# Performance work log

Measured on AMD Instinct MI355X. Metric: run time of the kernel, lower is better.

## Reference

```python
import jax, jax.numpy as jnp
import numpy as np

B, N = 1, 512
CS, CZ = 384, 128
H, DQK, DV, PQK, PV = 12, 16, 16, 4, 8
EPS = 1e-8
SW = float(np.sqrt(1.0 / (3 * DQK)))            # scalar_weights
PW = float(np.sqrt(1.0 / (3 * PQK * 9.0 / 2)))  # point_weights
ZW = float(np.sqrt(1.0 / 3))                    # attention_2d_weights


def _lin(key, din, dout):
    return 0.02 * jax.random.normal(key, (din, dout), dtype=jnp.float32), jnp.zeros((dout,), dtype=jnp.float32)


def setup_inputs():
    key = jax.random.key(0)
    ks = jax.random.split(key, 16)
    Wsq, bsq = _lin(ks[0], CS, H * DQK)
    Wsk, bsk = _lin(ks[1], CS, H * DQK)
    Wsv, bsv = _lin(ks[2], CS, H * DV)
    Wsb, bsb = _lin(ks[3], CZ, H)
    Wpq, bpq = _lin(ks[4], CS, H * PQK * 3)
    Wpk, bpk = _lin(ks[5], CS, H * PQK * 3)
    Wpv, bpv = _lin(ks[6], CS, H * PV * 3)
    Wout, bout = _lin(ks[7], H * (DV + PV * 4 + CZ), CS)
    w_attn = 0.5 * jax.random.normal(ks[8], (3,), dtype=jnp.float32)  # attn_linear weight (1,3)
    b_attn = jnp.zeros((), dtype=jnp.float32)
    tpw = jnp.full((H,), float(np.log(np.e - 1.0)), dtype=jnp.float32)  # trainable_point_weight
    s = jax.random.normal(ks[9], (B, N, CS), dtype=jnp.float32)
    z = jax.random.normal(ks[10], (B, N, N, CZ), dtype=jnp.float32)
    rot = jax.random.normal(ks[11], (B, N, 3, 3), dtype=jnp.float32)
    tran = jax.random.normal(ks[12], (B, N, 3), dtype=jnp.float32)
    res_mask = jnp.ones((B, N), dtype=jnp.float32)
    return dict(s=s, z=z, rot=rot, tran=tran, res_mask=res_mask,
                Wsq=Wsq, bsq=bsq, Wsk=Wsk, bsk=bsk, Wsv=Wsv, bsv=bsv,
                Wsb=Wsb, bsb=bsb, Wpq=Wpq, bpq=bpq, Wpk=Wpk, bpk=bpk,
                Wpv=Wpv, bpv=bpv, w_attn=w_attn, b_attn=b_attn, tpw=tpw,
                Wout=Wout, bout=bout)


def _ipa(s, z, rot, tran, res_mask, Wsq, bsq, Wsk, bsk, Wsv, bsv, Wsb, bsb,
         Wpq, bpq, Wpk, bpk, Wpv, bpv, w_attn, b_attn, tpw, Wout, bout):
    b, n, _ = s.shape
    sq = (s @ Wsq + bsq).reshape(b, n, H, DQK)
    sk = (s @ Wsk + bsk).reshape(b, n, H, DQK)
    sv = (s @ Wsv + bsv).reshape(b, n, H, DV)
    sb = z @ Wsb + bsb  # [b, i, j, h] pair bias

    def to_global(W, bias, p):
        t = (s @ W + bias).reshape(b, n, H, p, 3)
        return jnp.einsum('bnxy,bnhpy->bnhpx', rot, t) + tran[:, :, None, None, :]

    pqg = to_global(Wpq, bpq, PQK)
    pkg = to_global(Wpk, bpk, PQK)
    pvg = to_global(Wpv, bpv, PV)

    diff = pqg[:, :, None] - pkg[:, None, :]          # [b, i, j, h, p, 3]
    sdist = jnp.sum(diff * diff, axis=(-1, -2))       # [b, i, j, h]

    attn_point = -0.5 * jax.nn.softplus(tpw) * sdist * PW
    attn_scalar = jnp.einsum('bihd,bjhd->bijh', sq * SW, sk)
    attn_pair = sb * ZW
    # attn_linear(stack([scalar, point, pair], -1)).squeeze(-1)
    logits = attn_scalar * w_attn[0] + attn_point * w_attn[1] + attn_pair * w_attn[2] + b_attn

    mask2d = res_mask[:, :, None] * res_mask[:, None, :]
    logits = jnp.where(mask2d[..., None] == 0, jnp.finfo(logits.dtype).min, logits)
    attn = jax.nn.softmax(logits, axis=2)             # softmax over j

    r_scalar = jnp.einsum('bijh,bjhd->bihd', attn, sv)
    r_pt_g = jnp.einsum('bijh,bjhpc->bihpc', attn, pvg)
    # rotate back to local frame: R^T (x - t)
    r_pt = jnp.einsum('biyx,bihpy->bihpx', rot, r_pt_g - tran[:, :, None, None, :])
    r_norm = jnp.sqrt(jnp.sum(r_pt * r_pt, axis=-1) + EPS)  # [b, i, h, p]
    r_pair = jnp.einsum('bijh,bijc->bihc', attn, z)

    cat = jnp.concatenate([r_scalar, r_pt.reshape(b, n, H, PV * 3), r_norm, r_pair], axis=-1)
    return cat.reshape(b, n, -1) @ Wout + bout


def reference(s, z, rot, tran, res_mask, Wsq, bsq, Wsk, bsk, Wsv, bsv, Wsb, bsb,
              Wpq, bpq, Wpk, bpk, Wpv, bpv, w_attn, b_attn, tpw, Wout, bout):
    return _ipa(s, z, rot, tran, res_mask, Wsq, bsq, Wsk, bsk, Wsv, bsv, Wsb, bsb,
                Wpq, bpq, Wpk, bpk, Wpv, bpv, w_attn, b_attn, tpw, Wout, bout)
```

## Files before the change

### kernel.cpp

```cpp
#include <hip/hip_runtime.h>
#include <hip/hip_bf16.h>
#include <math.h>

#define NN 512
#define CSD 384
#define CZ 128
#define HH 12
#define TMPW 1152
#define CATH 176
#define CATDIM 2112
#define NSPLIT 6
#define KSPL 352

#define SW 0.14433756729740643f
#define PW 0.13608276348795434f
#define ZW 0.57735026918962576f
#define NEG_INF -3.4028234663852886e38f

typedef float f32x4_t __attribute__((ext_vector_type(4)));
typedef short bf16x8_t __attribute__((ext_vector_type(8)));

union BFU { uint4 q; bf16x8_t v; ushort u[8]; };

static __device__ __forceinline__ ushort f2bf(float f) {
    __hip_bfloat16 h = __float2bfloat16(f);
    return *reinterpret_cast<ushort*>(&h);
}
static __device__ __forceinline__ float bf2f(ushort u) {
    unsigned int v = ((unsigned int)u) << 16;
    return __uint_as_float(v);
}

__global__ void proj_gemm_kernel(const float* __restrict__ s, const float* __restrict__ rot,
                                 const float* __restrict__ tran,
                                 const float* __restrict__ Wsq, const float* __restrict__ bsq,
                                 const float* __restrict__ Wsk, const float* __restrict__ bsk,
                                 const float* __restrict__ Wsv, const float* __restrict__ bsv,
                                 const float* __restrict__ Wpq, const float* __restrict__ bpq,
                                 const float* __restrict__ Wpk, const float* __restrict__ bpk,
                                 const float* __restrict__ Wpv, const float* __restrict__ bpv,
                                 float* __restrict__ tmp)
{
    int bx = blockIdx.x;
    int n0 = blockIdx.y * 32;
    int f0 = bx * 48;
    const float* W; const float* bb; int dout; int segstart;
    if (bx < 4)       { W = Wsq; bb = bsq; dout = 192; segstart = 0; }
    else if (bx < 8)  { W = Wsk; bb = bsk; dout = 192; segstart = 192; }
    else if (bx < 12) { W = Wsv; bb = bsv; dout = 192; segstart = 384; }
    else if (bx < 15) { W = Wpq; bb = bpq; dout = 144; segstart = 576; }
    else if (bx < 18) { W = Wpk; bb = bpk; dout = 144; segstart = 720; }
    else              { W = Wpv; bb = bpv; dout = 288; segstart = 864; }
    int colbase = f0 - segstart;

    __shared__ float St[32][34];
    __shared__ float Ws[32][49];
    int tid = threadIdx.x;
    int ty = tid >> 4, tx = tid & 15;
    float acc[2][3] = {{0,0,0},{0,0,0}};

    for (int k0 = 0; k0 < CSD; k0 += 32) {
        {
            int r = tid >> 3, c4 = (tid & 7) * 4;
            float4 v = *(const float4*)&s[(size_t)(n0 + r) * CSD + k0 + c4];
            St[c4 + 0][r] = v.x; St[c4 + 1][r] = v.y; St[c4 + 2][r] = v.z; St[c4 + 3][r] = v.w;
        }
        for (int e = tid; e < 1536; e += 256) {
            int r = e / 48, c = e % 48;
            Ws[r][c] = W[(size_t)(k0 + r) * dout + colbase + c];
        }
        __syncthreads();
        #pragma unroll
        for (int k = 0; k < 32; k++) {
            float2 a = *(const float2*)&St[k][ty * 2];
            float b0 = Ws[k][tx * 3], b1 = Ws[k][tx * 3 + 1], b2 = Ws[k][tx * 3 + 2];
            acc[0][0] += a.x * b0; acc[0][1] += a.x * b1; acc[0][2] += a.x * b2;
            acc[1][0] += a.y * b0; acc[1][1] += a.y * b1; acc[1][2] += a.y * b2;
        }
        __syncthreads();
    }
    float bv0 = bb[colbase + tx * 3], bv1 = bb[colbase + tx * 3 + 1], bv2 = bb[colbase + tx * 3 + 2];
    #pragma unroll
    for (int r = 0; r < 2; r++) {
        int n = n0 + ty * 2 + r;
        float v0 = acc[r][0] + bv0, v1 = acc[r][1] + bv1, v2 = acc[r][2] + bv2;
        float* o = tmp + (size_t)n * TMPW + f0 + tx * 3;
        if (bx >= 12) {
            const float* R = rot + n * 9;
            const float* T = tran + n * 3;
            float g0 = R[0] * v0 + R[1] * v1 + R[2] * v2 + T[0];
            float g1 = R[3] * v0 + R[4] * v1 + R[5] * v2 + T[1];
            float g2 = R[6] * v0 + R[7] * v1 + R[8] * v2 + T[2];
            o[0] = g0; o[1] = g1; o[2] = g2;
        } else {
            o[0] = v0; o[1] = v1; o[2] = v2;
        }
    }
}

__global__ __launch_bounds__(512) void fused_z_kernel(const float* __restrict__ z,
                                                      const float* __restrict__ resm,
                                                      const float* __restrict__ Wsb,
                                                      const float* __restrict__ bsb,
                                                      const float* __restrict__ watt,
                                                      const float* __restrict__ batt,
                                                      const float* __restrict__ tpw,
                                                      const float* __restrict__ tmp,
                                                      ushort* __restrict__ attn_bf,
                                                      float* __restrict__ cat)
{
    int i = blockIdx.x;
    __shared__ float lt[NN * 17];
    __shared__ float sbz[NN * 12];
    __shared__ float sqs[192];
    __shared__ float pqi[144];
    __shared__ float cpt[12];
    __shared__ float cb[12];
    int tid = threadIdx.x;
    int w = tid >> 6, lane = tid & 63;
    int l16 = lane & 15, lhi = lane >> 4;
    float w0 = watt[0], w1 = watt[1], w2 = watt[2], ba = batt[0];
    float A2 = w2 * ZW;

    for (int k = tid; k < 192; k += 512) sqs[k] = tmp[(size_t)i * TMPW + k] * (SW * w0);
    if (tid < 144) pqi[tid] = tmp[(size_t)i * TMPW + 576 + tid];
    if (tid < 12) {
        cpt[tid] = -0.5f * log1pf(expf(tpw[tid])) * PW * w1;
        cb[tid]  = A2 * bsb[tid] + ba;
    }

    BFU breg[4];
    #pragma unroll
    for (int kk = 0; kk < 4; kk++) {
        #pragma unroll
        for (int e = 0; e < 8; e++) {
            int k = kk * 32 + lhi * 8 + e;
            float v = (l16 < HH) ? Wsb[k * HH + l16] * A2 : 0.f;
            breg[kk].u[e] = f2bf(v);
        }
    }

    const float* zi = z + (size_t)i * NN * CZ;
    float4 prA[8], prB[8];
    {
        const float* zr = zi + (size_t)(w * 16 + l16) * CZ + lhi * 8;
        #pragma unroll
        for (int kk = 0; kk < 4; kk++) {
            prA[kk * 2]     = *(const float4*)&zr[kk * 32];
            prA[kk * 2 + 1] = *(const float4*)&zr[kk * 32 + 4];
        }
    }
    #pragma unroll
    for (int t = 0; t < 4; t++) {
        float4* cur = (t & 1) ? prB : prA;
        float4* nxt = (t & 1) ? prA : prB;
        if (t < 3) {
            const float* zr = zi + (size_t)((w + 8 * (t + 1)) * 16 + l16) * CZ + lhi * 8;
            #pragma unroll
            for (int kk = 0; kk < 4; kk++) {
                nxt[kk * 2]     = *(const float4*)&zr[kk * 32];
                nxt[kk * 2 + 1] = *(const float4*)&zr[kk * 32 + 4];
            }
        }
        f32x4_t acc = {0.f, 0.f, 0.f, 0.f};
        #pragma unroll
        for (int kk = 0; kk < 4; kk++) {
            float4 f0 = cur[kk * 2], f1 = cur[kk * 2 + 1];
            BFU a;
            a.u[0] = f2bf(f0.x); a.u[1] = f2bf(f0.y); a.u[2] = f2bf(f0.z); a.u[3] = f2bf(f0.w);
            a.u[4] = f2bf(f1.x); a.u[5] = f2bf(f1.y); a.u[6] = f2bf(f1.z); a.u[7] = f2bf(f1.w);
            acc = __builtin_amdgcn_mfma_f32_16x16x32_bf16(a.v, breg[kk].v, acc, 0, 0, 0);
        }
        if (l16 < HH) {
            int T = w + 8 * t;
            #pragma unroll
            for (int r = 0; r < 4; r++)
                sbz[(T * 16 + lhi * 4 + r) * 12 + l16] = acc[r];
        }
    }
    __syncthreads();

    {
        int jg = tid >> 2, hg = tid & 3, h0 = hg * 3;
        float rmi = resm[i];
        #pragma unroll
        for (int rr = 0; rr < 4; rr++) {
            int j = jg + 128 * rr;
            float mj = rmi * resm[j];
            const float* sbr = &sbz[j * 12 + h0];
            #pragma unroll
            for (int t = 0; t < 3; t++) {
                int h = h0 + t;
                const float4* skp = (const float4*)(tmp + (size_t)j * TMPW + 192 + h * 16);
                const float4* sqp = (const float4*)&sqs[h * 16];
                float d0 = 0.f;
                #pragma unroll
                for (int q = 0; q < 4; q++) {
                    float4 kv = skp[q];
                    float4 qv = sqp[q];
                    d0 += qv.x * kv.x + qv.y * kv.y + qv.z * kv.z + qv.w * kv.w;
                }
                const float4* pkp = (const float4*)(tmp + (size_t)j * TMPW + 720 + h * 12);
                const float4* pqp = (const float4*)&pqi[h * 12];
                float sd = 0.f;
                #pragma unroll
                for (int q = 0; q < 3; q++) {
                    float4 kv = pkp[q];
                    float4 qv = pqp[q];
                    float a = qv.x - kv.x, bb2 = qv.y - kv.y, cc = qv.z - kv.z, e = qv.w - kv.w;
                    sd += a * a + bb2 * bb2 + cc * cc + e * e;
                }
                float lg = cb[h] + sbr[t] + d0 + cpt[h] * sd;
                if (mj == 0.f) lg = NEG_INF;
                lt[j * 17 + h] = lg;
            }
        }
    }
    __syncthreads();

    if (w < 4) {
        #pragma unroll
        for (int t = 0; t < 3; t++) {
            int h = w * 3 + t;
            float v[8]; float m = -INFINITY;
            #pragma unroll
            for (int u = 0; u < 8; u++) { v[u] = lt[(lane + 64 * u) * 17 + h]; m = fmaxf(m, v[u]); }
            for (int off = 32; off; off >>= 1) m = fmaxf(m, __shfl_xor(m, off));
            float ssum = 0.f;
            #pragma unroll
            for (int u = 0; u < 8; u++) { v[u] = __expf(v[u] - m); ssum += v[u]; }
            for (int off = 32; off; off >>= 1) ssum += __shfl_xor(ssum, off);
            float inv = 1.f / ssum;
            ushort* ag = attn_bf + ((size_t)i * HH + h) * NN;
            #pragma unroll
            for (int u = 0; u < 8; u++) {
                float p = v[u] * inv;
                lt[(lane + 64 * u) * 17 + h] = p;
                ag[lane + 64 * u] = f2bf(p);
            }
        }
    }
    __syncthreads();

    {
        int jq = w >> 1;
        int c = (w & 1) * 64 + lane;
        float acc[12];
        #pragma unroll
        for (int h = 0; h < 12; h++) acc[h] = 0.f;
        const float* zq = zi + (size_t)(jq * 128) * CZ + c;
        for (int j = 0; j < 128; j += 8) {
            float zv[8];
            #pragma unroll
            for (int u = 0; u < 8; u++) zv[u] = zq[(size_t)(j + u) * CZ];
            #pragma unroll
            for (int u = 0; u < 8; u++) {
                const float* pr = &lt[(jq * 128 + j + u) * 17];
                #pragma unroll
                for (int h = 0; h < 12; h++) acc[h] += pr[h] * zv[u];
            }
        }
        float* pslab = sbz;
        #pragma unroll
        for (int h = 0; h < 12; h++) pslab[(jq * 12 + h) * 128 + c] = acc[h];
    }
    __syncthreads();

    for (int e = tid; e < 1536; e += 512) {
        int h = e >> 7, c = e & 127;
        float ssum = sbz[h * 128 + c] + sbz[(12 + h) * 128 + c]
                   + sbz[(24 + h) * 128 + c] + sbz[(36 + h) * 128 + c];
        cat[(size_t)i * CATDIM + h * CATH + 48 + c] = ssum;
    }
}

__global__ void head_sum_kernel(const ushort* __restrict__ attn_bf, const float* __restrict__ tmp,
                                const float* __restrict__ rot, const float* __restrict__ tran,
                                float* __restrict__ cat)
{
    int i0 = blockIdx.x * 32;
    int h  = blockIdx.y;
    __shared__ float At[32][65];
    __shared__ float Sr[64][44];
    __shared__ float Rp[32][24];
    int tid = threadIdx.x;
    int il = tid & 31, fg = tid >> 5;
    float acc[5] = {0,0,0,0,0};

    for (int jc = 0; jc < NN; jc += 64) {
        {
            int r = tid >> 3, c8 = (tid & 7) * 8;
            const ushort* src = attn_bf + ((size_t)(i0 + r) * HH + h) * NN + jc + c8;
            BFU v; v.q = *(const uint4*)src;
            #pragma unroll
            for (int q = 0; q < 8; q++) At[r][c8 + q] = bf2f(v.u[q]);
        }
        {
            int jr = tid >> 2, d4 = (tid & 3) * 4;
            *(float4*)&Sr[jr][d4] = *(const float4*)&tmp[(size_t)(jc + jr) * TMPW + 384 + h * 16 + d4];
        }
        for (int e = tid; e < 384; e += 256) {
            int jr = e / 6, p4 = (e % 6) * 4;
            *(float4*)&Sr[jr][16 + p4] = *(const float4*)&tmp[(size_t)(jc + jr) * TMPW + 864 + h * 24 + p4];
        }
        __syncthreads();
        #pragma unroll 4
        for (int j = 0; j < 64; j++) {
            float a = At[il][j];
            #pragma unroll
            for (int q = 0; q < 5; q++) acc[q] += a * Sr[j][fg * 5 + q];
        }
        __syncthreads();
    }

    float* cbase = cat + (size_t)(i0 + il) * CATDIM + h * CATH;
    #pragma unroll
    for (int q = 0; q < 5; q++) {
        int f = fg * 5 + q;
        if (f < 16) cbase[f] = acc[q];
        else Rp[il][f - 16] = acc[q];
    }
    __syncthreads();

    {
        int il2 = tid >> 3, p = tid & 7;
        int i = i0 + il2;
        float gx = Rp[il2][p * 3 + 0] - tran[i * 3 + 0];
        float gy = Rp[il2][p * 3 + 1] - tran[i * 3 + 1];
        float gz = Rp[il2][p * 3 + 2] - tran[i * 3 + 2];
        const float* R = rot + i * 9;
        float lx = R[0] * gx + R[3] * gy + R[6] * gz;
        float ly = R[1] * gx + R[4] * gy + R[7] * gz;
        float lz = R[2] * gx + R[5] * gy + R[8] * gz;
        float nrm = sqrtf(lx * lx + ly * ly + lz * lz + 1e-8f);
        float* cp = cat + (size_t)i * CATDIM + h * CATH;
        cp[16 + p * 3 + 0] = lx; cp[16 + p * 3 + 1] = ly; cp[16 + p * 3 + 2] = lz;
        cp[40 + p] = nrm;
    }
}

__global__ void out_gemm_split_kernel(const float* __restrict__ cat, const float* __restrict__ Wout,
                                      float* __restrict__ part)
{
    int n0 = blockIdx.x * 64;
    int i0 = blockIdx.y * 64;
    int ks = blockIdx.z * KSPL;
    __shared__ float St[32][68];
    __shared__ float Bs[32][68];
    int tid = threadIdx.x;
    int ty = tid >> 4, tx = tid & 15;
    float acc[4][4] = {{0,0,0,0},{0,0,0,0},{0,0,0,0},{0,0,0,0}};

    for (int k0 = 0; k0 < KSPL; k0 += 32) {
        {
            int r = tid >> 2, c8 = (tid & 3) * 8;
            const float* src = cat + (size_t)(i0 + r) * CATDIM + ks + k0 + c8;
            float4 v0 = *(const float4*)src;
            float4 v1 = *(const float4*)(src + 4);
            St[c8+0][r]=v0.x; St[c8+1][r]=v0.y; St[c8+2][r]=v0.z; St[c8+3][r]=v0.w;
            St[c8+4][r]=v1.x; St[c8+5][r]=v1.y; St[c8+6][r]=v1.z; St[c8+7][r]=v1.w;
        }
        {
            int r = tid >> 3, c8 = (tid & 7) * 8;
            const float* src = Wout + (size_t)(ks + k0 + r) * CSD + n0 + c8;
            *(float4*)&Bs[r][c8]     = *(const float4*)src;
            *(float4*)&Bs[r][c8 + 4] = *(const float4*)(src + 4);
        }
        __syncthreads();
        #pragma unroll
        for (int k = 0; k < 32; k++) {
            float4 a = *(const float4*)&St[k][ty * 4];
            float4 b = *(const float4*)&Bs[k][tx * 4];
            float av[4] = {a.x, a.y, a.z, a.w};
            float bv[4] = {b.x, b.y, b.z, b.w};
            #pragma unroll
            for (int r = 0; r < 4; r++)
                #pragma unroll
                for (int c = 0; c < 4; c++) acc[r][c] += av[r] * bv[c];
        }
        __syncthreads();
    }
    #pragma unroll
    for (int r = 0; r < 4; r++) {
        float4 v = make_float4(acc[r][0], acc[r][1], acc[r][2], acc[r][3]);
        *(float4*)&part[((size_t)blockIdx.z * NN + i0 + ty * 4 + r) * CSD + n0 + tx * 4] = v;
    }
}

__global__ void reduce_out_kernel(const float* __restrict__ part, const float* __restrict__ bout,
                                  float* __restrict__ out)
{
    int v = blockIdx.x * 256 + threadIdx.x;
    int n4 = v % 96;
    float4 o = ((const float4*)bout)[n4];
    const float4* p4 = (const float4*)part;
    #pragma unroll
    for (int s = 0; s < NSPLIT; s++) {
        float4 t = p4[(size_t)s * 49152 + v];
        o.x += t.x; o.y += t.y; o.z += t.z; o.w += t.w;
    }
    ((float4*)out)[v] = o;
}

extern "C" void kernel_launch(void* const* d_in, const int* in_sizes, int n_in,
                              void* d_out, int out_size, void* d_ws, size_t ws_size,
                              hipStream_t stream) {
    const float* s    = (const float*)d_in[0];
    const float* z    = (const float*)d_in[1];
    const float* rot  = (const float*)d_in[2];
    const float* tran = (const float*)d_in[3];
    const float* resm = (const float*)d_in[4];
    const float* Wsq  = (const float*)d_in[5];  const float* bsq = (const float*)d_in[6];
    const float* Wsk  = (const float*)d_in[7];  const float* bsk = (const float*)d_in[8];
    const float* Wsv  = (const float*)d_in[9];  const float* bsv = (const float*)d_in[10];
    const float* Wsb  = (const float*)d_in[11]; const float* bsb = (const float*)d_in[12];
    const float* Wpq  = (const float*)d_in[13]; const float* bpq = (const float*)d_in[14];
    const float* Wpk  = (const float*)d_in[15]; const float* bpk = (const float*)d_in[16];
    const float* Wpv  = (const float*)d_in[17]; const float* bpv = (const float*)d_in[18];
    const float* watt = (const float*)d_in[19]; const float* batt = (const float*)d_in[20];
    const float* tpw  = (const float*)d_in[21];
    const float* Wout = (const float*)d_in[22]; const float* bout = (const float*)d_in[23];
    float* out = (float*)d_out;
    float* ws  = (float*)d_ws;

    float*  tmp     = ws;
    ushort* attn_bf = (ushort*)(ws + 589824);
    float*  cat     = ws + 589824 + 1572864;
    float*  partO   = cat + 1081344;

    proj_gemm_kernel<<<dim3(24, 16), 256, 0, stream>>>(s, rot, tran,
                                                       Wsq, bsq, Wsk, bsk, Wsv, bsv,
                                                       Wpq, bpq, Wpk, bpk, Wpv, bpv, tmp);
    fused_z_kernel<<<512, 512, 0, stream>>>(z, resm, Wsb, bsb, watt, batt, tpw,
                                            tmp, attn_bf, cat);
    head_sum_kernel<<<dim3(16, 12), 256, 0, stream>>>(attn_bf, tmp, rot, tran, cat);
    out_gemm_split_kernel<<<dim3(6, 8, NSPLIT), 256, 0, stream>>>(cat, Wout, partO);
    reduce_out_kernel<<<192, 256, 0, stream>>>(partO, bout, out);
}
```

Measured before the change: 182.3 us.

## Split fused z kernel into logits/softmax and pair-reduction kernels

The single 512-thread z kernel becomes two 256-thread kernels. The first computes the pair bias with MFMA and folds the logit computation directly onto the MFMA accumulator registers, which removes the sbz shared buffer and one barrier. The second reads the bf16 attention weights back and reduces them against z using float2 loads. Smaller shared memory and launch bounds of (256, 4) aim for higher occupancy. The cost is reading z twice from memory, about 128MB in total, and using bf16-rounded attention for r_pair.

```diff
diff --git a/kernel.cpp b/kernel.cpp
--- a/kernel.cpp
+++ b/kernel.cpp
@@ -98,22 +98,17 @@
     }
 }
 
-__global__ __launch_bounds__(512) void fused_z_kernel(const float* __restrict__ z,
-                                                      const float* __restrict__ resm,
-                                                      const float* __restrict__ Wsb,
-                                                      const float* __restrict__ bsb,
-                                                      const float* __restrict__ watt,
-                                                      const float* __restrict__ batt,
-                                                      const float* __restrict__ tpw,
-                                                      const float* __restrict__ tmp,
-                                                      ushort* __restrict__ attn_bf,
-                                                      float* __restrict__ cat)
+__global__ __launch_bounds__(256, 4) void sbz_logits_softmax_kernel(
+        const float* __restrict__ z, const float* __restrict__ resm,
+        const float* __restrict__ Wsb, const float* __restrict__ bsb,
+        const float* __restrict__ watt, const float* __restrict__ batt,
+        const float* __restrict__ tpw, const float* __restrict__ tmp,
+        ushort* __restrict__ attn_bf)
 {
     int i = blockIdx.x;
     __shared__ float lt[NN * 17];
-    __shared__ float sbz[NN * 12];
-    __shared__ float sqs[192];
-    __shared__ float pqi[144];
+    __shared__ float sqs[12 * 24];
+    __shared__ float pqi[12 * 24];
     __shared__ float cpt[12];
     __shared__ float cb[12];
     int tid = threadIdx.x;
@@ -122,8 +117,14 @@
     float w0 = watt[0], w1 = watt[1], w2 = watt[2], ba = batt[0];
     float A2 = w2 * ZW;
 
-    for (int k = tid; k < 192; k += 512) sqs[k] = tmp[(size_t)i * TMPW + k] * (SW * w0);
-    if (tid < 144) pqi[tid] = tmp[(size_t)i * TMPW + 576 + tid];
+    if (tid < 192) {
+        int h = tid >> 4, d = tid & 15;
+        sqs[h * 24 + d] = tmp[(size_t)i * TMPW + tid] * (SW * w0);
+    }
+    if (tid < 144) {
+        int h = tid / 12, d = tid % 12;
+        pqi[h * 24 + d] = tmp[(size_t)i * TMPW + 576 + tid];
+    }
     if (tid < 12) {
         cpt[tid] = -0.5f * log1pf(expf(tpw[tid])) * PW * w1;
         cb[tid]  = A2 * bsb[tid] + ba;
@@ -139,8 +140,13 @@
             breg[kk].u[e] = f2bf(v);
         }
     }
+    __syncthreads();
 
     const float* zi = z + (size_t)i * NN * CZ;
+    float rmi = resm[i];
+    float cpth = cpt[l16 < HH ? l16 : 0];
+    float cbh  = cb[l16 < HH ? l16 : 0];
+
     float4 prA[8], prB[8];
     {
         const float* zr = zi + (size_t)(w * 16 + l16) * CZ + lhi * 8;
@@ -150,12 +156,12 @@
             prA[kk * 2 + 1] = *(const float4*)&zr[kk * 32 + 4];
         }
     }
-    #pragma unroll
-    for (int t = 0; t < 4; t++) {
+
+    for (int t = 0; t < 8; t++) {
         float4* cur = (t & 1) ? prB : prA;
         float4* nxt = (t & 1) ? prA : prB;
-        if (t < 3) {
-            const float* zr = zi + (size_t)((w + 8 * (t + 1)) * 16 + l16) * CZ + lhi * 8;
+        if (t < 7) {
+            const float* zr = zi + (size_t)((w + 4 * (t + 1)) * 16 + l16) * CZ + lhi * 8;
             #pragma unroll
             for (int kk = 0; kk < 4; kk++) {
                 nxt[kk * 2]     = *(const float4*)&zr[kk * 32];
@@ -172,27 +178,15 @@
             acc = __builtin_amdgcn_mfma_f32_16x16x32_bf16(a.v, breg[kk].v, acc, 0, 0, 0);
         }
         if (l16 < HH) {
-            int T = w + 8 * t;
-            #pragma unroll
-            for (int r = 0; r < 4; r++)
-                sbz[(T * 16 + lhi * 4 + r) * 12 + l16] = acc[r];
-        }
-    }
-    __syncthreads();
-
-    {
-        int jg = tid >> 2, hg = tid & 3, h0 = hg * 3;
-        float rmi = resm[i];
-        #pragma unroll
-        for (int rr = 0; rr < 4; rr++) {
-            int j = jg + 128 * rr;
-            float mj = rmi * resm[j];
-            const float* sbr = &sbz[j * 12 + h0];
-            #pragma unroll
-            for (int t = 0; t < 3; t++) {
-                int h = h0 + t;
+            int h = l16;
+            int jbase = (w + 4 * t) * 16;
+            const float4* sqp = (const float4*)&sqs[h * 24];
+            const float4* pqp = (const float4*)&pqi[h * 24];
+            #pragma unroll
+            for (int r = 0; r < 4; r++) {
+                int j = jbase + lhi * 4 + r;
+                float mj = rmi * resm[j];
                 const float4* skp = (const float4*)(tmp + (size_t)j * TMPW + 192 + h * 16);
-                const float4* sqp = (const float4*)&sqs[h * 16];
                 float d0 = 0.f;
                 #pragma unroll
                 for (int q = 0; q < 4; q++) {
@@ -201,7 +195,6 @@
                     d0 += qv.x * kv.x + qv.y * kv.y + qv.z * kv.z + qv.w * kv.w;
                 }
                 const float4* pkp = (const float4*)(tmp + (size_t)j * TMPW + 720 + h * 12);
-                const float4* pqp = (const float4*)&pqi[h * 12];
                 float sd = 0.f;
                 #pragma unroll
                 for (int q = 0; q < 3; q++) {
@@ -210,7 +203,7 @@
                     float a = qv.x - kv.x, bb2 = qv.y - kv.y, cc = qv.z - kv.z, e = qv.w - kv.w;
                     sd += a * a + bb2 * bb2 + cc * cc + e * e;
                 }
-                float lg = cb[h] + sbr[t] + d0 + cpt[h] * sd;
+                float lg = cbh + acc[r] + d0 + cpth * sd;
                 if (mj == 0.f) lg = NEG_INF;
                 lt[j * 17 + h] = lg;
             }
@@ -218,58 +211,80 @@
     }
     __syncthreads();
 
-    if (w < 4) {
-        #pragma unroll
-        for (int t = 0; t < 3; t++) {
-            int h = w * 3 + t;
-            float v[8]; float m = -INFINITY;
-            #pragma unroll
-            for (int u = 0; u < 8; u++) { v[u] = lt[(lane + 64 * u) * 17 + h]; m = fmaxf(m, v[u]); }
-            for (int off = 32; off; off >>= 1) m = fmaxf(m, __shfl_xor(m, off));
-            float ssum = 0.f;
-            #pragma unroll
-            for (int u = 0; u < 8; u++) { v[u] = __expf(v[u] - m); ssum += v[u]; }
-            for (int off = 32; off; off >>= 1) ssum += __shfl_xor(ssum, off);
-            float inv = 1.f / ssum;
-            ushort* ag = attn_bf + ((size_t)i * HH + h) * NN;
-            #pragma unroll
-            for (int u = 0; u < 8; u++) {
-                float p = v[u] * inv;
-                lt[(lane + 64 * u) * 17 + h] = p;
-                ag[lane + 64 * u] = f2bf(p);
+    #pragma unroll
+    for (int t = 0; t < 3; t++) {
+        int h = w * 3 + t;
+        float v[8]; float m = -INFINITY;
+        #pragma unroll
+        for (int u = 0; u < 8; u++) { v[u] = lt[(lane + 64 * u) * 17 + h]; m = fmaxf(m, v[u]); }
+        for (int off = 32; off; off >>= 1) m = fmaxf(m, __shfl_xor(m, off));
+        float ssum = 0.f;
+        #pragma unroll
+        for (int u = 0; u < 8; u++) { v[u] = __expf(v[u] - m); ssum += v[u]; }
+        for (int off = 32; off; off >>= 1) ssum += __shfl_xor(ssum, off);
+        float inv = 1.f / ssum;
+        ushort* ag = attn_bf + ((size_t)i * HH + h) * NN;
+        #pragma unroll
+        for (int u = 0; u < 8; u++) ag[lane + 64 * u] = f2bf(v[u] * inv);
+    }
+}
+
+__global__ __launch_bounds__(256, 4) void rpair_kernel(const float* __restrict__ z,
+                                                       const ushort* __restrict__ attn_bf,
+                                                       float* __restrict__ cat)
+{
+    int i = blockIdx.x;
+    __shared__ ushort pbf[NN * 12];
+    __shared__ float pslab[4 * 12 * 128];
+    int tid = threadIdx.x;
+
+    for (int e = tid; e < 768; e += 256) {
+        int h = e >> 6, g = e & 63;
+        BFU v; v.q = *(const uint4*)&attn_bf[((size_t)i * HH + h) * NN + g * 8];
+        #pragma unroll
+        for (int q = 0; q < 8; q++) pbf[(g * 8 + q) * 12 + h] = v.u[q];
+    }
+    __syncthreads();
+
+    int w = tid >> 6, lane = tid & 63;
+    int c0 = lane * 2;
+    const float* zq = z + ((size_t)i * NN + w * 128) * CZ + c0;
+    float acc[12][2];
+    #pragma unroll
+    for (int h = 0; h < 12; h++) { acc[h][0] = 0.f; acc[h][1] = 0.f; }
+
+    for (int j0 = 0; j0 < 128; j0 += 16) {
+        float2 zv[16];
+        #pragma unroll
+        for (int u = 0; u < 16; u++) zv[u] = *(const float2*)&zq[(size_t)(j0 + u) * CZ];
+        #pragma unroll
+        for (int u = 0; u < 16; u++) {
+            int j = w * 128 + j0 + u;
+            const uint2* pr = (const uint2*)&pbf[j * 12];
+            uint2 pa = pr[0], pb2 = pr[1], pc = pr[2];
+            float ph[12];
+            ph[0]  = bf2f((ushort)(pa.x & 0xffff)); ph[1]  = bf2f((ushort)(pa.x >> 16));
+            ph[2]  = bf2f((ushort)(pa.y & 0xffff)); ph[3]  = bf2f((ushort)(pa.y >> 16));
+            ph[4]  = bf2f((ushort)(pb2.x & 0xffff)); ph[5]  = bf2f((ushort)(pb2.x >> 16));
+            ph[6]  = bf2f((ushort)(pb2.y & 0xffff)); ph[7]  = bf2f((ushort)(pb2.y >> 16));
+            ph[8]  = bf2f((ushort)(pc.x & 0xffff)); ph[9]  = bf2f((ushort)(pc.x >> 16));
+            ph[10] = bf2f((ushort)(pc.y & 0xffff)); ph[11] = bf2f((ushort)(pc.y >> 16));
+            #pragma unroll
+            for (int h = 0; h < 12; h++) {
+                acc[h][0] += ph[h] * zv[u].x;
+                acc[h][1] += ph[h] * zv[u].y;
             }
         }
     }
+    #pragma unroll
+    for (int h = 0; h < 12; h++)
+        *(float2*)&pslab[(w * 12 + h) * 128 + c0] = make_float2(acc[h][0], acc[h][1]);
     __syncthreads();
 
-    {
-        int jq = w >> 1;
-        int c = (w & 1) * 64 + lane;
-        float acc[12];
-        #pragma unroll
-        for (int h = 0; h < 12; h++) acc[h] = 0.f;
-        const float* zq = zi + (size_t)(jq * 128) * CZ + c;
-        for (int j = 0; j < 128; j += 8) {
-            float zv[8];
-            #pragma unroll
-            for (int u = 0; u < 8; u++) zv[u] = zq[(size_t)(j + u) * CZ];
-            #pragma unroll
-            for (int u = 0; u < 8; u++) {
-                const float* pr = &lt[(jq * 128 + j + u) * 17];
-                #pragma unroll
-                for (int h = 0; h < 12; h++) acc[h] += pr[h] * zv[u];
-            }
-        }
-        float* pslab = sbz;
-        #pragma unroll
-        for (int h = 0; h < 12; h++) pslab[(jq * 12 + h) * 128 + c] = acc[h];
-    }
-    __syncthreads();
-
-    for (int e = tid; e < 1536; e += 512) {
+    for (int e = tid; e < 1536; e += 256) {
         int h = e >> 7, c = e & 127;
-        float ssum = sbz[h * 128 + c] + sbz[(12 + h) * 128 + c]
-                   + sbz[(24 + h) * 128 + c] + sbz[(36 + h) * 128 + c];
+        float ssum = pslab[h * 128 + c] + pslab[(12 + h) * 128 + c]
+                   + pslab[(24 + h) * 128 + c] + pslab[(36 + h) * 128 + c];
         cat[(size_t)i * CATDIM + h * CATH + 48 + c] = ssum;
     }
 }
@@ -431,8 +446,9 @@
     proj_gemm_kernel<<<dim3(24, 16), 256, 0, stream>>>(s, rot, tran,
                                                        Wsq, bsq, Wsk, bsk, Wsv, bsv,
                                                        Wpq, bpq, Wpk, bpk, Wpv, bpv, tmp);
-    fused_z_kernel<<<512, 512, 0, stream>>>(z, resm, Wsb, bsb, watt, batt, tpw,
-                                            tmp, attn_bf, cat);
+    sbz_logits_softmax_kernel<<<512, 256, 0, stream>>>(z, resm, Wsb, bsb, watt, batt,
+                                                       tpw, tmp, attn_bf);
+    rpair_kernel<<<512, 256, 0, stream>>>(z, attn_bf, cat);
     head_sum_kernel<<<dim3(16, 12), 256, 0, stream>>>(attn_bf, tmp, rot, tran, cat);
     out_gemm_split_kernel<<<dim3(6, 8, NSPLIT), 256, 0, stream>>>(cat, Wout, partO);
     reduce_out_kernel<<<192, 256, 0, stream>>>(partO, bout, out);
```

Result: slower. 267.1 us (+46.5%).
